# Performance work log

Measured on AMD Instinct MI355X. Metric: run time of the kernel, lower is better.

Reference implementation:

```python
import jax, jax.numpy as jnp
import numpy as np
from jax import lax

N_QUBITS = 10
N_LAYERS = 6
DIM = 1 << N_QUBITS
EPS = 1e-5

_i = np.arange(DIM)
# Z_SIGNS[w, i] = (+1/-1) eigenvalue of PauliZ on wire w (wire 0 = most significant bit)
Z_SIGNS = jnp.asarray(np.stack([1.0 - 2.0 * ((_i >> (N_QUBITS - 1 - w)) & 1) for w in range(N_QUBITS)]).astype(np.float32))

def _layer_perm(r):
    # composed permutation of the ring of CNOT(w, (w+r)%n) gates of one StronglyEntanglingLayers layer
    p = _i.copy()
    for w in range(N_QUBITS):
        c, t = w, (w + r) % N_QUBITS
        pc, pt = N_QUBITS - 1 - c, N_QUBITS - 1 - t
        pg = _i ^ (((_i >> pc) & 1) << pt)
        p = p[pg]
    return p

LAYER_PERMS = [jnp.asarray(_layer_perm(l % (N_QUBITS - 1) + 1), dtype=jnp.int32) for l in range(N_LAYERS)]

def _apply_1q(state, U, wire):
    # state: (B, DIM) complex64; U: (2,2) or batched (B,2,2)
    B = state.shape[0]
    left = 1 << wire
    right = DIM // (2 * left)
    s = state.reshape(B, left, 2, right)
    if U.ndim == 3:
        out = jnp.einsum('bij,bljr->blir', U, s)
    else:
        out = jnp.einsum('ij,bljr->blir', U, s)
    return out.reshape(B, DIM)

def _ry_batched(theta):
    c = jnp.cos(theta / 2)
    s = jnp.sin(theta / 2)
    return jnp.stack([jnp.stack([c, -s], -1), jnp.stack([s, c], -1)], -2).astype(jnp.complex64)

def _rot(phi, theta, omega):
    # PennyLane Rot(phi, theta, omega) = RZ(omega) @ RY(theta) @ RZ(phi)
    c = jnp.cos(theta / 2)
    s = jnp.sin(theta / 2)
    m00 = jnp.exp(-1j * (phi + omega) / 2) * c
    m01 = -jnp.exp(1j * (phi - omega) / 2) * s
    m10 = jnp.exp(-1j * (phi - omega) / 2) * s
    m11 = jnp.exp(1j * (phi + omega) / 2) * c
    return jnp.stack([jnp.stack([m00, m01]), jnp.stack([m10, m11])]).astype(jnp.complex64)

def quantum_forward(xq, qw):
    # batched statevector simulation of: RY(pi*x_i) encoding + StronglyEntanglingLayers
    B = xq.shape[0]
    state = jnp.zeros((B, DIM), jnp.complex64).at[:, 0].set(1.0)
    for w in range(N_QUBITS):
        state = _apply_1q(state, _ry_batched(jnp.pi * xq[:, w]), w)
    for l in range(N_LAYERS):
        for w in range(N_QUBITS):
            state = _apply_1q(state, _rot(qw[l, w, 0], qw[l, w, 1], qw[l, w, 2]), w)
        state = state[:, LAYER_PERMS[l]]
    probs = state.real ** 2 + state.imag ** 2
    return probs @ Z_SIGNS.T  # (B, N_QUBITS) expvals of PauliZ

def _conv(x, w, b):
    y = lax.conv_general_dilated(x, w, (1, 1), 'SAME', dimension_numbers=('NCHW', 'OIHW', 'NCHW'))
    return y + b[None, :, None, None]

def _bn(x, g, b):
    # BatchNorm2d in training mode: per-batch statistics over (N, H, W)
    m = jnp.mean(x, (0, 2, 3), keepdims=True)
    v = jnp.var(x, (0, 2, 3), keepdims=True)
    return (x - m) * lax.rsqrt(v + EPS) * g[None, :, None, None] + b[None, :, None, None]

def _pool(x):
    return lax.reduce_window(x, -jnp.inf, lax.max, (1, 1, 2, 2), (1, 1, 2, 2), 'VALID')

def setup_inputs() -> dict:
    key = jax.random.key(0)
    ks = jax.random.split(key, 16)
    n = lambda k, sh, sc: jax.random.normal(k, sh, jnp.float32) * sc
    return {
        'x': jax.random.normal(ks[0], (256, 3, 64, 64), jnp.float32),
        'conv1_w': n(ks[1], (32, 3, 3, 3), 0.1), 'conv1_b': jnp.zeros(32),
        'bn1_g': jnp.ones(32), 'bn1_b': jnp.zeros(32),
        'conv2_w': n(ks[2], (32, 32, 3, 3), 0.05), 'conv2_b': jnp.zeros(32),
        'bn2_g': jnp.ones(32), 'bn2_b': jnp.zeros(32),
        'conv3_w': n(ks[3], (64, 32, 3, 3), 0.05), 'conv3_b': jnp.zeros(64),
        'bn3_g': jnp.ones(64), 'bn3_b': jnp.zeros(64),
        'conv4_w': n(ks[4], (64, 64, 3, 3), 0.05), 'conv4_b': jnp.zeros(64),
        'bn4_g': jnp.ones(64), 'bn4_b': jnp.zeros(64),
        'fc1_w': n(ks[5], (128, 64 * 16 * 16), 0.01), 'fc1_b': jnp.zeros(128),
        'fc2_w': n(ks[6], (10, 128), 0.05), 'fc2_b': jnp.zeros(10),
        'q_weights': jax.random.uniform(ks[7], (6, 10, 3), jnp.float32),
        'head_w': n(ks[8], (10, 10), 0.1), 'head_b': jnp.zeros(10),
    }

def reference(x, conv1_w, conv1_b, bn1_g, bn1_b, conv2_w, conv2_b, bn2_g, bn2_b,
              conv3_w, conv3_b, bn3_g, bn3_b, conv4_w, conv4_b, bn4_g, bn4_b,
              fc1_w, fc1_b, fc2_w, fc2_b, q_weights, head_w, head_b):
    h = jax.nn.relu(_bn(_conv(x, conv1_w, conv1_b), bn1_g, bn1_b))
    h = jax.nn.relu(_bn(_conv(h, conv2_w, conv2_b), bn2_g, bn2_b))
    h = _pool(h)  # Dropout(0.25) is identity in eval
    h = jax.nn.relu(_bn(_conv(h, conv3_w, conv3_b), bn3_g, bn3_b))
    h = jax.nn.relu(_bn(_conv(h, conv4_w, conv4_b), bn4_g, bn4_b))
    h = _pool(h)
    h = h.reshape(h.shape[0], -1)  # (B, 64*16*16)
    h = jax.nn.relu(h @ fc1_w.T + fc1_b)
    h = h @ fc2_w.T + fc2_b  # (B, n_qubits)
    q = quantum_forward(h, q_weights)
    return q @ head_w.T + head_b  # (B, num_classes)
```

## Files before the change

kernel.cpp:

```cpp
#include <hip/hip_runtime.h>
#include <math.h>

#define PI_F 3.14159265358979323846f

typedef __attribute__((ext_vector_type(8))) _Float16 half8;
typedef __attribute__((ext_vector_type(4))) _Float16 half4;
typedef __attribute__((ext_vector_type(4))) float f32x4;

__global__ __launch_bounds__(256) void x_to_nhwc4_kernel(
    const float* __restrict__ x, _Float16* __restrict__ X4)
{
    int idx = blockIdx.x * 256 + threadIdx.x;
    int n = idx >> 11;
    int p = (idx & 2047) * 2;
    const float* xb = x + (size_t)n * 12288;
    float2 c0 = *(const float2*)&xb[p];
    float2 c1 = *(const float2*)&xb[4096 + p];
    float2 c2 = *(const float2*)&xb[8192 + p];
    half8 o;
    o[0] = (_Float16)c0.x; o[1] = (_Float16)c1.x; o[2] = (_Float16)c2.x; o[3] = (_Float16)0.f;
    o[4] = (_Float16)c0.y; o[5] = (_Float16)c1.y; o[6] = (_Float16)c2.y; o[7] = (_Float16)0.f;
    *(half8*)&X4[(size_t)idx * 8] = o;
}

__global__ __launch_bounds__(256) void wt_transform_kernel(
    const float* __restrict__ w1, const float* __restrict__ w2,
    const float* __restrict__ w3, const float* __restrict__ w4,
    _Float16* __restrict__ t1, _Float16* __restrict__ t2,
    _Float16* __restrict__ t3, _Float16* __restrict__ t4)
{
    int idx = blockIdx.x * 256 + threadIdx.x;
    if (idx < 9216) {
        int j = idx & 7, co = (idx >> 3) & 31, k8 = idx >> 8;
        int k = k8 * 8 + j, tap = k >> 5, ci = k & 31;
        t2[idx] = (_Float16)w2[(size_t)(co * 32 + ci) * 9 + tap];
    } else if (idx < 27648) {
        int e = idx - 9216;
        int j = e & 7, co = (e >> 3) & 31, r = e >> 8;
        int k8 = r % 36, gg = r / 36;
        int k = k8 * 8 + j, tap = k >> 5, ci = k & 31;
        t3[e] = (_Float16)w3[(size_t)((gg * 32 + co) * 32 + ci) * 9 + tap];
    } else if (idx < 64512) {
        int e = idx - 27648;
        int j = e & 7, co = (e >> 3) & 31, r = e >> 8;
        int k8 = r % 36, gc = r / 36;
        int g = gc >> 1, cc = gc & 1;
        int kl = k8 * 8 + j, tap = kl >> 5, ci = cc * 32 + (kl & 31);
        t4[e] = (_Float16)w4[(size_t)((g * 32 + co) * 64 + ci) * 9 + tap];
    } else if (idx < 66560) {
        int e = idx - 64512;
        int j = e & 7, co = (e >> 3) & 31, k8 = e >> 8;
        int k = k8 * 8 + j, tap = k >> 2, ci = k & 3;
        t1[e] = (_Float16)((tap < 9 && ci < 3) ? w1[(size_t)(co * 3 + ci) * 9 + tap] : 0.f);
    }
}

__global__ __launch_bounds__(256) void fc1w_transform_kernel(
    const float* __restrict__ w, _Float16* __restrict__ wt)
{
    __shared__ float lds[64][65];
    const int t = threadIdx.x;
    const int yx0 = blockIdx.x * 64;
    const int j = blockIdx.y;
    #pragma unroll
    for (int i = 0; i < 16; ++i) {
        int idx = t + 256 * i;
        int c = idx >> 6, yxl = idx & 63;
        lds[c][yxl] = w[(size_t)j * 16384 + c * 256 + yx0 + yxl];
    }
    __syncthreads();
    #pragma unroll
    for (int i = 0; i < 2; ++i) {
        int idx = t + 256 * i;
        int yxl = idx >> 3, c8 = idx & 7;
        half8 h;
        #pragma unroll
        for (int jj = 0; jj < 8; ++jj)
            h[jj] = (_Float16)lds[c8 * 8 + jj][yxl];
        *(half8*)&wt[(size_t)j * 16384 + (size_t)(yx0 + yxl) * 64 + c8 * 8] = h;
    }
}

__global__ __launch_bounds__(256) void quantum_prep_kernel(
    const float* __restrict__ qw, float* __restrict__ rotm,
    unsigned short* __restrict__ perm)
{
    int t = threadIdx.x;
    if (t < 60) {
        float phi = qw[t * 3], th = qw[t * 3 + 1], om = qw[t * 3 + 2];
        float c = cosf(0.5f * th), s = sinf(0.5f * th);
        float apo = 0.5f * (phi + om), amo = 0.5f * (phi - om);
        float cpo = cosf(apo), spo = sinf(apo);
        float cmo = cosf(amo), smo = sinf(amo);
        rotm[t * 8 + 0] = cpo * c;  rotm[t * 8 + 1] = -spo * c;
        rotm[t * 8 + 2] = -cmo * s; rotm[t * 8 + 3] = -smo * s;
        rotm[t * 8 + 4] = cmo * s;  rotm[t * 8 + 5] = -smo * s;
        rotm[t * 8 + 6] = cpo * c;  rotm[t * 8 + 7] = spo * c;
    }
    for (int e = t; e < 6144; e += 256) {
        int layer = e >> 10, i = e & 1023;
        int r = layer % 9 + 1;
        int jdx = i;
        for (int w = 9; w >= 0; --w) {
            int tt = (w + r) % 10;
            int pc = 9 - w, pt_ = 9 - tt;
            jdx ^= ((jdx >> pc) & 1) << pt_;
        }
        perm[e] = (unsigned short)jdx;
    }
}

__global__ __launch_bounds__(256) void conv1_mfma_kernel(
    const _Float16* __restrict__ X4, const _Float16* __restrict__ w1m,
    const float* __restrict__ bias, _Float16* __restrict__ out,
    float* __restrict__ partials)
{
    constexpr int TC = 66, TR = 6;
    constexpr int NPIX = (TR + 1) * TC;
    __shared__ __align__(16) _Float16 s_in[NPIX * 4];
    __shared__ __align__(16) _Float16 s_w[2048];
    __shared__ float s_red[64];

    const int t = threadIdx.x;
    const int row0 = blockIdx.x * 4;
    const int n = blockIdx.z;

    *(half8*)&s_w[t * 8] = *(const half8*)&w1m[t * 8];

    for (int p = t; p < NPIX; p += 256) {
        int col = p % TC, r = p / TC;
        int gy = row0 + r - 1, gx = col - 1;
        uint2 u = make_uint2(0u, 0u);
        if (r < TR && gy >= 0 && gy < 64 && gx >= 0 && gx < 64)
            u = *(const uint2*)&X4[(((size_t)n << 12) + (gy << 6) + gx) * 4];
        *(uint2*)&s_in[p * 4] = u;
    }
    if (t < 64) s_red[t] = 0.f;
    __syncthreads();

    const int w = t >> 6, l = t & 63;
    const int lm = l & 15, lg = l >> 4;
    int pA[4];
    #pragma unroll
    for (int f = 0; f < 4; ++f) {
        int m = w * 64 + f * 16 + lm;
        pA[f] = (m >> 6) * TC + (m & 63);
    }
    f32x4 zero4 = {0.f, 0.f, 0.f, 0.f};
    f32x4 acc[4][2];
    #pragma unroll
    for (int f = 0; f < 4; ++f) { acc[f][0] = zero4; acc[f][1] = zero4; }

    {
        const int t0 = lg * 2;
        const int off0 = (t0 / 3) * TC + (t0 % 3);
        const int off1 = ((t0 + 1) / 3) * TC + ((t0 + 1) % 3);
        half8 b0 = *(const half8*)&s_w[(lg * 32 + lm) * 8];
        half8 b1 = *(const half8*)&s_w[(lg * 32 + 16 + lm) * 8];
        #pragma unroll
        for (int f = 0; f < 4; ++f) {
            half4 alo = *(const half4*)&s_in[(pA[f] + off0) * 4];
            half4 ahi = *(const half4*)&s_in[(pA[f] + off1) * 4];
            half8 a;
            #pragma unroll
            for (int j = 0; j < 4; ++j) { a[j] = alo[j]; a[4 + j] = ahi[j]; }
            acc[f][0] = __builtin_amdgcn_mfma_f32_16x16x32_f16(a, b0, acc[f][0], 0, 0, 0);
            acc[f][1] = __builtin_amdgcn_mfma_f32_16x16x32_f16(a, b1, acc[f][1], 0, 0, 0);
        }
    }
    {
        half8 b0 = *(const half8*)&s_w[((4 + lg) * 32 + lm) * 8];
        half8 b1 = *(const half8*)&s_w[((4 + lg) * 32 + 16 + lm) * 8];
        #pragma unroll
        for (int f = 0; f < 4; ++f) {
            half8 a;
            #pragma unroll
            for (int j = 0; j < 8; ++j) a[j] = (_Float16)0.f;
            if (lg == 0) {
                half4 alo = *(const half4*)&s_in[(pA[f] + 134) * 4];
                half4 ahi = *(const half4*)&s_in[(pA[f] + 198) * 4];
                #pragma unroll
                for (int j = 0; j < 4; ++j) { a[j] = alo[j]; a[4 + j] = ahi[j]; }
            }
            acc[f][0] = __builtin_amdgcn_mfma_f32_16x16x32_f16(a, b0, acc[f][0], 0, 0, 0);
            acc[f][1] = __builtin_amdgcn_mfma_f32_16x16x32_f16(a, b1, acc[f][1], 0, 0, 0);
        }
    }

    float bv0 = bias[lm];
    float bv1 = bias[16 + lm];
    float s0 = 0.f, s20 = 0.f, s1 = 0.f, s21 = 0.f;
    #pragma unroll
    for (int f = 0; f < 4; ++f) {
        #pragma unroll
        for (int r = 0; r < 4; ++r) {
            int m = w * 64 + f * 16 + lg * 4 + r;
            int yy = row0 + (m >> 6), xo = m & 63;
            size_t base = (((size_t)n * 64 + yy) * 64 + xo) * 32;
            float v0 = acc[f][0][r] + bv0;
            float v1 = acc[f][1][r] + bv1;
            out[base + lm] = (_Float16)v0;
            out[base + 16 + lm] = (_Float16)v1;
            s0 += v0; s20 += v0 * v0;
            s1 += v1; s21 += v1 * v1;
        }
    }
    s0 += __shfl_xor(s0, 16);  s0 += __shfl_xor(s0, 32);
    s1 += __shfl_xor(s1, 16);  s1 += __shfl_xor(s1, 32);
    s20 += __shfl_xor(s20, 16); s20 += __shfl_xor(s20, 32);
    s21 += __shfl_xor(s21, 16); s21 += __shfl_xor(s21, 32);
    if (l < 16) {
        atomicAdd(&s_red[lm], s0);
        atomicAdd(&s_red[16 + lm], s1);
        atomicAdd(&s_red[32 + lm], s20);
        atomicAdd(&s_red[48 + lm], s21);
    }
    __syncthreads();
    if (t < 64)
        partials[((size_t)n * 16 + blockIdx.x) * 64 + t] = s_red[t];
}

template<int BLOCK, int W, int CIN, int COUT, int NCH, int MF, int NB,
         bool MMIN, bool POOL>
__global__ __launch_bounds__(BLOCK, (BLOCK == 512 ? 4 : 3)) void conv_mfma_kernel(
    const _Float16* __restrict__ in0, const _Float16* __restrict__ in1,
    const _Float16* __restrict__ coef, const _Float16* __restrict__ wt,
    const float* __restrict__ bias,
    _Float16* __restrict__ out0, _Float16* __restrict__ out1,
    float* __restrict__ partials)
{
    constexpr int H = W;
    constexpr int NWAVE = BLOCK / 64;
    constexpr int SPW = MF * 16;
    constexpr int ROWS = NWAVE * SPW / W;
    constexpr int TR = ROWS + 2;
    constexpr int TC = W + 2;
    constexpr int NPIX = TR * TC;
    constexpr int CCI = 32;
    constexpr int KC = 9 * CCI;
    constexpr int COUTB = NB * 16;
    __shared__ __align__(16) _Float16 s_in[NPIX * CCI];
    __shared__ float s_red[2 * COUTB];

    const int t = threadIdx.x;
    const int row0 = blockIdx.x * ROWS;
    const int n = blockIdx.z;

    const int w = t >> 6, l = t & 63;
    const int lm = l & 15, lg = l >> 4;
    int pA[MF];
    #pragma unroll
    for (int f = 0; f < MF; ++f) {
        int m = w * SPW + f * 16 + lm;
        pA[f] = (m / W) * TC + (m % W);
    }
    f32x4 zero4 = {0.f, 0.f, 0.f, 0.f};
    f32x4 acc[MF][NB];
    #pragma unroll
    for (int f = 0; f < MF; ++f)
        #pragma unroll
        for (int nb = 0; nb < NB; ++nb) acc[f][nb] = zero4;
    if (t < 2 * COUTB) s_red[t] = 0.f;

    #pragma unroll
    for (int cc = 0; cc < NCH; ++cc) {
        __syncthreads();
        for (int idx = t; idx < NPIX * 4; idx += BLOCK) {
            int c8 = idx & 3;
            int p = idx >> 2;
            int col = p % TC, r = p / TC;
            int gy = row0 + r - 1, gx = col - 1;
            half8 v;
            #pragma unroll
            for (int j = 0; j < 8; ++j) v[j] = (_Float16)0.f;
            if (gy >= 0 && gy < H && gx >= 0 && gx < W) {
                size_t gidx = (((size_t)n * H + gy) * W + gx) * CIN + cc * CCI + c8 * 8;
                if (MMIN) {
                    half8 mn = *(const half8*)&in0[gidx];
                    half8 mx = *(const half8*)&in1[gidx];
                    half8 sa = *(const half8*)&coef[cc * CCI + c8 * 8];
                    half8 sb = *(const half8*)&coef[CIN + cc * CCI + c8 * 8];
                    half8 sh = *(const half8*)&coef[2 * CIN + cc * CCI + c8 * 8];
                    #pragma unroll
                    for (int j = 0; j < 8; ++j) {
                        _Float16 f = mx[j] * sa[j] + mn[j] * sb[j] + sh[j];
                        v[j] = f > (_Float16)0.f ? f : (_Float16)0.f;
                    }
                } else {
                    v = *(const half8*)&in0[gidx];
                    if (coef) {
                        half8 sc = *(const half8*)&coef[cc * CCI + c8 * 8];
                        half8 sh = *(const half8*)&coef[CIN + cc * CCI + c8 * 8];
                        #pragma unroll
                        for (int j = 0; j < 8; ++j) {
                            _Float16 f = v[j] * sc[j] + sh[j];
                            v[j] = f > (_Float16)0.f ? f : (_Float16)0.f;
                        }
                    }
                }
            }
            *(half8*)&s_in[(c8 * NPIX + p) * 8] = v;
        }
        __syncthreads();
        #pragma unroll
        for (int tap = 0; tap < 9; ++tap) {
            const int dy = tap / 3, dx = tap % 3;
            const int poff = dy * TC + dx;
            half8 b[NB];
            #pragma unroll
            for (int nb = 0; nb < NB; ++nb) {
                int cog = nb * 16 + lm;
                int gg = cog >> 5, col = cog & 31;
                const _Float16* wp = wt + (size_t)(gg * NCH + cc) * KC * 32;
                b[nb] = *(const half8*)&wp[((tap * 4 + lg) * 32 + col) * 8];
            }
            #pragma unroll
            for (int f = 0; f < MF; ++f) {
                half8 a = *(const half8*)&s_in[(lg * NPIX + pA[f] + poff) * 8];
                #pragma unroll
                for (int nb = 0; nb < NB; ++nb)
                    acc[f][nb] = __builtin_amdgcn_mfma_f32_16x16x32_f16(a, b[nb], acc[f][nb], 0, 0, 0);
            }
        }
    }

    float bv[NB], s[NB], s2[NB];
    #pragma unroll
    for (int nb = 0; nb < NB; ++nb) {
        bv[nb] = bias[nb * 16 + lm];
        s[nb] = 0.f; s2[nb] = 0.f;
    }
    #pragma unroll
    for (int f = 0; f < MF; ++f) {
        #pragma unroll
        for (int r = 0; r < 4; ++r) {
            int m = w * SPW + f * 16 + lg * 4 + r;
            int yy = row0 + m / W, xo = m % W;
            size_t base = (((size_t)n * H + yy) * W + xo) * COUT;
            #pragma unroll
            for (int nb = 0; nb < NB; ++nb) {
                float v = acc[f][nb][r] + bv[nb];
                if (!POOL) out0[base + nb * 16 + lm] = (_Float16)v;
                s[nb] += v; s2[nb] += v * v;
            }
        }
    }
    #pragma unroll
    for (int nb = 0; nb < NB; ++nb) {
        s[nb] += __shfl_xor(s[nb], 16);  s[nb] += __shfl_xor(s[nb], 32);
        s2[nb] += __shfl_xor(s2[nb], 16); s2[nb] += __shfl_xor(s2[nb], 32);
    }
    if (l < 16) {
        #pragma unroll
        for (int nb = 0; nb < NB; ++nb) {
            atomicAdd(&s_red[nb * 16 + lm], s[nb]);
            atomicAdd(&s_red[COUTB + nb * 16 + lm], s2[nb]);
        }
    }

    if (POOL) {
        constexpr int FH = MF / 2;
        const int yp = (row0 >> 1) + w;
        #pragma unroll
        for (int nb = 0; nb < NB; ++nb) {
            #pragma unroll
            for (int f = 0; f < FH; ++f) {
                #pragma unroll
                for (int rp = 0; rp < 2; ++rp) {
                    float a0 = acc[f][nb][2 * rp] + bv[nb];
                    float a1 = acc[f][nb][2 * rp + 1] + bv[nb];
                    float a2 = acc[f + FH][nb][2 * rp] + bv[nb];
                    float a3 = acc[f + FH][nb][2 * rp + 1] + bv[nb];
                    float mn = fminf(fminf(a0, a1), fminf(a2, a3));
                    float mx = fmaxf(fmaxf(a0, a1), fmaxf(a2, a3));
                    int xp = f * 8 + lg * 2 + rp;
                    size_t ob = (((size_t)n * (W / 2) + yp) * (W / 2) + xp) * COUT
                                + nb * 16 + lm;
                    out0[ob] = (_Float16)mn;
                    out1[ob] = (_Float16)mx;
                }
            }
        }
    }

    __syncthreads();
    if (t < 2 * COUTB) {
        size_t bid = (size_t)n * gridDim.x + blockIdx.x;
        partials[bid * 2 * COUTB + t] = s_red[t];
    }
}

__global__ __launch_bounds__(256) void bn_finalize_kernel(
    const float* __restrict__ partials, int nx, float inv_count,
    const float* __restrict__ gamma, const float* __restrict__ beta,
    float* __restrict__ ss, _Float16* __restrict__ ssh,
    _Float16* __restrict__ sab, int COUT)
{
    const int c = blockIdx.x;
    const int t = threadIdx.x;
    float sum = 0.f, sq = 0.f;
    int total = 256 * nx;
    for (int e = t; e < total; e += 256) {
        size_t off = (size_t)e * 2 * COUT;
        sum += partials[off + c];
        sq  += partials[off + COUT + c];
    }
    #pragma unroll
    for (int off = 32; off > 0; off >>= 1) {
        sum += __shfl_xor(sum, off);
        sq  += __shfl_xor(sq, off);
    }
    __shared__ float rs[4], rq[4];
    if ((t & 63) == 0) { rs[t >> 6] = sum; rq[t >> 6] = sq; }
    __syncthreads();
    if (t == 0) {
        sum = rs[0] + rs[1] + rs[2] + rs[3];
        sq  = rq[0] + rq[1] + rq[2] + rq[3];
        float mean = sum * inv_count;
        float var = sq * inv_count - mean * mean;
        float scale = gamma[c] * rsqrtf(var + 1e-5f);
        float shift = beta[c] - mean * scale;
        ss[c] = scale;
        ss[COUT + c] = shift;
        if (ssh) {
            ssh[c] = (_Float16)scale;
            ssh[COUT + c] = (_Float16)shift;
        }
        if (sab) {
            sab[c] = (_Float16)(scale > 0.f ? scale : 0.f);
            sab[COUT + c] = (_Float16)(scale > 0.f ? 0.f : scale);
            sab[2 * COUT + c] = (_Float16)shift;
        }
    }
}

__global__ __launch_bounds__(256) void fc1_mfma_kernel(
    const _Float16* __restrict__ Amin, const _Float16* __restrict__ Amax,
    const _Float16* __restrict__ sab, const _Float16* __restrict__ Bw,
    float* __restrict__ hp)
{
    __shared__ __align__(16) _Float16 As[64][72];
    __shared__ __align__(16) _Float16 Bs[128][72];
    const int t = threadIdx.x;
    const int mt = blockIdx.x;
    const int kc = blockIdx.y;
    const int w = t >> 6, l = t & 63;
    const int lm = l & 15, lg = l >> 4;

    f32x4 zero4 = {0.f, 0.f, 0.f, 0.f};
    f32x4 acc[8];
    #pragma unroll
    for (int nb = 0; nb < 8; ++nb) acc[nb] = zero4;

    const size_t a_base = (size_t)(mt * 64) * 16384 + (size_t)kc * 512;
    const size_t b_base = (size_t)kc * 512;

    for (int p = 0; p < 8; ++p) {
        __syncthreads();
        #pragma unroll
        for (int i = 0; i < 2; ++i) {
            int idx = t + 256 * i;
            int r = idx >> 3, c8 = idx & 7;
            size_t off = a_base + (size_t)r * 16384 + p * 64 + c8 * 8;
            half8 mn = *(const half8*)&Amin[off];
            half8 mx = *(const half8*)&Amax[off];
            half8 sa = *(const half8*)&sab[c8 * 8];
            half8 sb = *(const half8*)&sab[64 + c8 * 8];
            half8 sh = *(const half8*)&sab[128 + c8 * 8];
            half8 v;
            #pragma unroll
            for (int j = 0; j < 8; ++j) {
                _Float16 f = mx[j] * sa[j] + mn[j] * sb[j] + sh[j];
                v[j] = f > (_Float16)0.f ? f : (_Float16)0.f;
            }
            *(half8*)&As[r][c8 * 8] = v;
        }
        #pragma unroll
        for (int i = 0; i < 4; ++i) {
            int idx = t + 256 * i;
            int r = idx >> 3, c8 = idx & 7;
            *(half8*)&Bs[r][c8 * 8] =
                *(const half8*)&Bw[b_base + (size_t)r * 16384 + p * 64 + c8 * 8];
        }
        __syncthreads();
        #pragma unroll
        for (int ks = 0; ks < 64; ks += 32) {
            half8 a = *(const half8*)&As[w * 16 + lm][ks + lg * 8];
            #pragma unroll
            for (int nb = 0; nb < 8; ++nb) {
                half8 b = *(const half8*)&Bs[nb * 16 + lm][ks + lg * 8];
                acc[nb] = __builtin_amdgcn_mfma_f32_16x16x32_f16(a, b, acc[nb], 0, 0, 0);
            }
        }
    }
    #pragma unroll
    for (int nb = 0; nb < 8; ++nb) {
        #pragma unroll
        for (int r = 0; r < 4; ++r) {
            int row = mt * 64 + w * 16 + lg * 4 + r;
            hp[((size_t)kc * 256 + row) * 128 + nb * 16 + lm] = acc[nb][r];
        }
    }
}

__global__ __launch_bounds__(256) void fc1_reduce_kernel(
    const float* __restrict__ hp, const float* __restrict__ bias, float* __restrict__ h1)
{
    int gid = blockIdx.x * 256 + threadIdx.x;
    int n = gid >> 7, j = gid & 127;
    float s = bias[j];
    #pragma unroll
    for (int kc = 0; kc < 32; ++kc) s += hp[((size_t)kc * 256 + n) * 128 + j];
    h1[gid] = fmaxf(0.f, s);
}

__global__ __launch_bounds__(64) void fc2_kernel(
    const float* __restrict__ h1, const float* __restrict__ w,
    const float* __restrict__ b, float* __restrict__ xq)
{
    int n = blockIdx.x, l = threadIdx.x;
    float a0 = h1[n * 128 + l], a1 = h1[n * 128 + 64 + l];
    float p[10];
    #pragma unroll
    for (int j = 0; j < 10; ++j)
        p[j] = w[j * 128 + l] * a0 + w[j * 128 + 64 + l] * a1;
    #pragma unroll
    for (int j = 0; j < 10; ++j) {
        #pragma unroll
        for (int off = 32; off > 0; off >>= 1) p[j] += __shfl_xor(p[j], off);
    }
    if (l == 0) {
        #pragma unroll
        for (int j = 0; j < 10; ++j) xq[n * 10 + j] = p[j] + b[j];
    }
}

__global__ __launch_bounds__(64) void quantum_head_kernel(
    const float* __restrict__ xq, const float* __restrict__ rotm,
    const unsigned short* __restrict__ perm,
    const float* __restrict__ head_w, const float* __restrict__ head_b,
    float* __restrict__ outp)
{
    __shared__ float lds[2048];
    const int n = blockIdx.x;
    const int l = threadIdx.x;

    float ar[16], ai[16];
    #pragma unroll
    for (int r = 0; r < 16; ++r) { ar[r] = 0.f; ai[r] = 0.f; }
    if (l == 0) ar[0] = 1.f;

    #pragma unroll
    for (int w = 0; w < 10; ++w) {
        float th = 0.5f * PI_F * xq[n * 10 + w];
        float c = cosf(th), s = sinf(th);
        const int k = 9 - w;
        if (k >= 6) {
            const int b = k - 6;
            #pragma unroll
            for (int r = 0; r < 16; ++r) {
                if (!(r & (1 << b))) {
                    int r1 = r | (1 << b);
                    float a0 = ar[r], a1 = ar[r1];
                    ar[r]  = c * a0 - s * a1;
                    ar[r1] = s * a0 + c * a1;
                }
            }
        } else {
            float ss = ((l >> k) & 1) ? s : -s;
            #pragma unroll
            for (int r = 0; r < 16; ++r) {
                float p = __shfl_xor(ar[r], 1 << k);
                ar[r] = c * ar[r] + ss * p;
            }
        }
    }

    #pragma unroll 1
    for (int layer = 0; layer < 6; ++layer) {
        #pragma unroll
        for (int w = 0; w < 10; ++w) {
            const float* m = rotm + (layer * 10 + w) * 8;
            float m00r = m[0], m00i = m[1], m01r = m[2], m01i = m[3];
            float m10r = m[4], m10i = m[5], m11r = m[6], m11i = m[7];
            const int k = 9 - w;
            if (k >= 6) {
                const int b = k - 6;
                #pragma unroll
                for (int r = 0; r < 16; ++r) {
                    if (!(r & (1 << b))) {
                        int r1 = r | (1 << b);
                        float a0r = ar[r], a0i = ai[r];
                        float a1r = ar[r1], a1i = ai[r1];
                        ar[r]  = m00r * a0r - m00i * a0i + m01r * a1r - m01i * a1i;
                        ai[r]  = m00r * a0i + m00i * a0r + m01r * a1i + m01i * a1r;
                        ar[r1] = m10r * a0r - m10i * a0i + m11r * a1r - m11i * a1i;
                        ai[r1] = m10r * a0i + m10i * a0r + m11r * a1i + m11i * a1r;
                    }
                }
            } else {
                int bit = (l >> k) & 1;
                float mAr = bit ? m11r : m00r, mAi = bit ? m11i : m00i;
                float mBr = bit ? m10r : m01r, mBi = bit ? m10i : m01i;
                #pragma unroll
                for (int r = 0; r < 16; ++r) {
                    float pr = __shfl_xor(ar[r], 1 << k);
                    float pi = __shfl_xor(ai[r], 1 << k);
                    float mr = ar[r], mi = ai[r];
                    ar[r] = mAr * mr - mAi * mi + mBr * pr - mBi * pi;
                    ai[r] = mAr * mi + mAi * mr + mBr * pi + mBi * pr;
                }
            }
        }
        #pragma unroll
        for (int r = 0; r < 16; ++r) {
            lds[(r << 6) | l] = ar[r];
            lds[1024 + ((r << 6) | l)] = ai[r];
        }
        __syncthreads();
        const unsigned short* pt = perm + layer * 1024;
        #pragma unroll
        for (int r = 0; r < 16; ++r) {
            int ji = pt[(r << 6) | l];
            ar[r] = lds[ji];
            ai[r] = lds[1024 + ji];
        }
        __syncthreads();
    }

    float S = 0.f, T0 = 0.f, T1 = 0.f, T2 = 0.f, T3 = 0.f;
    #pragma unroll
    for (int r = 0; r < 16; ++r) {
        float pr = ar[r] * ar[r] + ai[r] * ai[r];
        S += pr;
        T0 += (r & 1) ? -pr : pr;
        T1 += (r & 2) ? -pr : pr;
        T2 += (r & 4) ? -pr : pr;
        T3 += (r & 8) ? -pr : pr;
    }
    float pk[10];
    pk[0] = T3; pk[1] = T2; pk[2] = T1; pk[3] = T0;
    #pragma unroll
    for (int w = 4; w < 10; ++w)
        pk[w] = ((l >> (9 - w)) & 1) ? -S : S;
    #pragma unroll
    for (int w = 0; w < 10; ++w) {
        #pragma unroll
        for (int off = 1; off < 64; off <<= 1)
            pk[w] += __shfl_xor(pk[w], off);
    }
    if (l < 10) {
        float o = head_b[l];
        #pragma unroll
        for (int kk = 0; kk < 10; ++kk) o += pk[kk] * head_w[l * 10 + kk];
        outp[n * 10 + l] = o;
    }
}

extern "C" void kernel_launch(void* const* d_in, const int* in_sizes, int n_in,
                              void* d_out, int out_size, void* d_ws, size_t ws_size,
                              hipStream_t stream)
{
    const float* x   = (const float*)d_in[0];
    const float* c1w = (const float*)d_in[1];  const float* c1b = (const float*)d_in[2];
    const float* g1  = (const float*)d_in[3];  const float* b1  = (const float*)d_in[4];
    const float* c2w = (const float*)d_in[5];  const float* c2b = (const float*)d_in[6];
    const float* g2  = (const float*)d_in[7];  const float* b2  = (const float*)d_in[8];
    const float* c3w = (const float*)d_in[9];  const float* c3b = (const float*)d_in[10];
    const float* g3  = (const float*)d_in[11]; const float* b3  = (const float*)d_in[12];
    const float* c4w = (const float*)d_in[13]; const float* c4b = (const float*)d_in[14];
    const float* g4  = (const float*)d_in[15]; const float* b4  = (const float*)d_in[16];
    const float* f1w = (const float*)d_in[17]; const float* f1b = (const float*)d_in[18];
    const float* f2w = (const float*)d_in[19]; const float* f2b = (const float*)d_in[20];
    const float* qw  = (const float*)d_in[21];
    const float* hw  = (const float*)d_in[22]; const float* hb  = (const float*)d_in[23];

    float* ws = (float*)d_ws;
    _Float16* H0 = (_Float16*)ws;
    _Float16* H1 = H0 + 33554432;
    float* part = ws + 33554432;
    float* ss1  = part + 524288;
    float* ss2  = ss1 + 64;
    float* ss3  = ss2 + 64;
    float* ss4  = ss3 + 128;
    float* hp   = ss4 + 128;
    float* h1   = hp + 1048576;
    float* xqv  = h1 + 32768;
    float* rotm = xqv + 2560;
    unsigned short* perm16 = (unsigned short*)(rotm + 480);
    _Float16* ssh1 = (_Float16*)(perm16 + 6144);
    _Float16* ssh3 = ssh1 + 64;
    _Float16* sab2 = ssh3 + 128;
    _Float16* sab4 = sab2 + 96;
    _Float16* wt2  = sab4 + 192;
    _Float16* wt3  = wt2 + 9216;
    _Float16* wt4  = wt3 + 18432;
    _Float16* w1m  = wt4 + 36864;
    _Float16* w1t  = w1m + 2048;
    _Float16* X4   = w1t + 2097152;

    _Float16* minT2 = H1;
    _Float16* maxT2 = H1 + 8388608;
    _Float16* minT4 = H1;
    _Float16* maxT4 = H1 + 4194304;

    quantum_prep_kernel<<<1, 256, 0, stream>>>(qw, rotm, perm16);
    wt_transform_kernel<<<260, 256, 0, stream>>>(c1w, c2w, c3w, c4w, w1m, wt2, wt3, wt4);
    fc1w_transform_kernel<<<dim3(4, 128), 256, 0, stream>>>(f1w, w1t);
    x_to_nhwc4_kernel<<<2048, 256, 0, stream>>>(x, X4);

    conv1_mfma_kernel<<<dim3(16, 1, 256), 256, 0, stream>>>(X4, w1m, c1b, H0, part);
    bn_finalize_kernel<<<32, 256, 0, stream>>>(part, 16, 1.f / 1048576.f,
                                               g1, b1, ss1, ssh1, nullptr, 32);

    conv_mfma_kernel<256, 64, 32, 32, 1, 8, 2, false, true>
        <<<dim3(8, 1, 256), 256, 0, stream>>>(
        H0, nullptr, ssh1, wt2, c2b, minT2, maxT2, part);
    bn_finalize_kernel<<<32, 256, 0, stream>>>(part, 8, 1.f / 1048576.f,
                                               g2, b2, ss2, nullptr, sab2, 32);

    conv_mfma_kernel<512, 32, 32, 64, 1, 4, 4, true, false>
        <<<dim3(2, 1, 256), 512, 0, stream>>>(
        minT2, maxT2, sab2, wt3, c3b, H0, nullptr, part);
    bn_finalize_kernel<<<64, 256, 0, stream>>>(part, 2, 1.f / 262144.f,
                                               g3, b3, ss3, ssh3, nullptr, 64);

    conv_mfma_kernel<512, 32, 64, 64, 2, 4, 4, false, true>
        <<<dim3(2, 1, 256), 512, 0, stream>>>(
        H0, nullptr, ssh3, wt4, c4b, minT4, maxT4, part);
    bn_finalize_kernel<<<64, 256, 0, stream>>>(part, 2, 1.f / 262144.f,
                                               g4, b4, ss4, nullptr, sab4, 64);

    fc1_mfma_kernel<<<dim3(4, 32), 256, 0, stream>>>(minT4, maxT4, sab4, w1t, hp);
    fc1_reduce_kernel<<<128, 256, 0, stream>>>(hp, f1b, h1);

    fc2_kernel<<<256, 64, 0, stream>>>(h1, f2w, f2b, xqv);

    quantum_head_kernel<<<256, 64, 0, stream>>>(xqv, rotm, perm16, hw, hb, (float*)d_out);
}
```

Measured before the change: 220.8 us.

## Stage all input channels once per conv block and coalesce pooled output stores via LDS

The conv kernel now loads every input channel of the halo tile into shared memory in a single pass, instead of looping over 32-channel chunks with a barrier pair per chunk. The MFMA loop is reordered to iterate taps then channel chunks. For pooled layers, min/max results are first packed into shared memory and then written out as contiguous half8 vectors, replacing scattered 2-byte global stores. The cost is more LDS per block for the CIN=64 case (conv4), which may lower occupancy, plus an extra barrier pair for the pooling pack.

```diff
diff --git a/kernel.cpp b/kernel.cpp
--- a/kernel.cpp
+++ b/kernel.cpp
@@ -220,7 +220,7 @@
         partials[((size_t)n * 16 + blockIdx.x) * 64 + t] = s_red[t];
 }
 
-template<int BLOCK, int W, int CIN, int COUT, int NCH, int MF, int NB,
+template<int BLOCK, int W, int CIN, int COUT, int MF, int NB,
          bool MMIN, bool POOL>
 __global__ __launch_bounds__(BLOCK, (BLOCK == 512 ? 4 : 3)) void conv_mfma_kernel(
     const _Float16* __restrict__ in0, const _Float16* __restrict__ in1,
@@ -236,10 +236,11 @@
     constexpr int TR = ROWS + 2;
     constexpr int TC = W + 2;
     constexpr int NPIX = TR * TC;
-    constexpr int CCI = 32;
-    constexpr int KC = 9 * CCI;
+    constexpr int NCH = CIN / 32;
+    constexpr int C8N = CIN / 8;
+    constexpr int KC = 288;
     constexpr int COUTB = NB * 16;
-    __shared__ __align__(16) _Float16 s_in[NPIX * CCI];
+    __shared__ __align__(16) _Float16 s_in[NPIX * CIN];
     __shared__ float s_red[2 * COUTB];
 
     const int t = threadIdx.x;
@@ -262,50 +263,50 @@
         for (int nb = 0; nb < NB; ++nb) acc[f][nb] = zero4;
     if (t < 2 * COUTB) s_red[t] = 0.f;
 
-    #pragma unroll
-    for (int cc = 0; cc < NCH; ++cc) {
-        __syncthreads();
-        for (int idx = t; idx < NPIX * 4; idx += BLOCK) {
-            int c8 = idx & 3;
-            int p = idx >> 2;
-            int col = p % TC, r = p / TC;
-            int gy = row0 + r - 1, gx = col - 1;
-            half8 v;
-            #pragma unroll
-            for (int j = 0; j < 8; ++j) v[j] = (_Float16)0.f;
-            if (gy >= 0 && gy < H && gx >= 0 && gx < W) {
-                size_t gidx = (((size_t)n * H + gy) * W + gx) * CIN + cc * CCI + c8 * 8;
-                if (MMIN) {
-                    half8 mn = *(const half8*)&in0[gidx];
-                    half8 mx = *(const half8*)&in1[gidx];
-                    half8 sa = *(const half8*)&coef[cc * CCI + c8 * 8];
-                    half8 sb = *(const half8*)&coef[CIN + cc * CCI + c8 * 8];
-                    half8 sh = *(const half8*)&coef[2 * CIN + cc * CCI + c8 * 8];
+    for (int idx = t; idx < NPIX * C8N; idx += BLOCK) {
+        int c8 = idx % C8N;
+        int p = idx / C8N;
+        int col = p % TC, r = p / TC;
+        int gy = row0 + r - 1, gx = col - 1;
+        half8 v;
+        #pragma unroll
+        for (int j = 0; j < 8; ++j) v[j] = (_Float16)0.f;
+        if (gy >= 0 && gy < H && gx >= 0 && gx < W) {
+            size_t gidx = (((size_t)n * H + gy) * W + gx) * CIN + c8 * 8;
+            if (MMIN) {
+                half8 mn = *(const half8*)&in0[gidx];
+                half8 mx = *(const half8*)&in1[gidx];
+                half8 sa = *(const half8*)&coef[c8 * 8];
+                half8 sb = *(const half8*)&coef[CIN + c8 * 8];
+                half8 sh = *(const half8*)&coef[2 * CIN + c8 * 8];
+                #pragma unroll
+                for (int j = 0; j < 8; ++j) {
+                    _Float16 f = mx[j] * sa[j] + mn[j] * sb[j] + sh[j];
+                    v[j] = f > (_Float16)0.f ? f : (_Float16)0.f;
+                }
+            } else {
+                v = *(const half8*)&in0[gidx];
+                if (coef) {
+                    half8 sc = *(const half8*)&coef[c8 * 8];
+                    half8 sh = *(const half8*)&coef[CIN + c8 * 8];
                     #pragma unroll
                     for (int j = 0; j < 8; ++j) {
-                        _Float16 f = mx[j] * sa[j] + mn[j] * sb[j] + sh[j];
+                        _Float16 f = v[j] * sc[j] + sh[j];
                         v[j] = f > (_Float16)0.f ? f : (_Float16)0.f;
                     }
-                } else {
-                    v = *(const half8*)&in0[gidx];
-                    if (coef) {
-                        half8 sc = *(const half8*)&coef[cc * CCI + c8 * 8];
-                        half8 sh = *(const half8*)&coef[CIN + cc * CCI + c8 * 8];
-                        #pragma unroll
-                        for (int j = 0; j < 8; ++j) {
-                            _Float16 f = v[j] * sc[j] + sh[j];
-                            v[j] = f > (_Float16)0.f ? f : (_Float16)0.f;
-                        }
-                    }
                 }
             }
-            *(half8*)&s_in[(c8 * NPIX + p) * 8] = v;
-        }
-        __syncthreads();
-        #pragma unroll
-        for (int tap = 0; tap < 9; ++tap) {
-            const int dy = tap / 3, dx = tap % 3;
-            const int poff = dy * TC + dx;
+        }
+        *(half8*)&s_in[(c8 * NPIX + p) * 8] = v;
+    }
+    __syncthreads();
+
+    #pragma unroll
+    for (int tap = 0; tap < 9; ++tap) {
+        const int dy = tap / 3, dx = tap % 3;
+        const int poff = dy * TC + dx;
+        #pragma unroll
+        for (int cc = 0; cc < NCH; ++cc) {
             half8 b[NB];
             #pragma unroll
             for (int nb = 0; nb < NB; ++nb) {
@@ -316,7 +317,7 @@
             }
             #pragma unroll
             for (int f = 0; f < MF; ++f) {
-                half8 a = *(const half8*)&s_in[(lg * NPIX + pA[f] + poff) * 8];
+                half8 a = *(const half8*)&s_in[((cc * 4 + lg) * NPIX + pA[f] + poff) * 8];
                 #pragma unroll
                 for (int nb = 0; nb < NB; ++nb)
                     acc[f][nb] = __builtin_amdgcn_mfma_f32_16x16x32_f16(a, b[nb], acc[f][nb], 0, 0, 0);
@@ -360,7 +361,10 @@
 
     if (POOL) {
         constexpr int FH = MF / 2;
-        const int yp = (row0 >> 1) + w;
+        constexpr int PPIX = (ROWS / 2) * (W / 2);
+        static_assert(2 * PPIX * COUT <= NPIX * CIN, "pool pack fits in s_in");
+        __syncthreads();
+        _Float16* pk = s_in;
         #pragma unroll
         for (int nb = 0; nb < NB; ++nb) {
             #pragma unroll
@@ -374,12 +378,17 @@
                     float mn = fminf(fminf(a0, a1), fminf(a2, a3));
                     float mx = fmaxf(fmaxf(a0, a1), fmaxf(a2, a3));
                     int xp = f * 8 + lg * 2 + rp;
-                    size_t ob = (((size_t)n * (W / 2) + yp) * (W / 2) + xp) * COUT
-                                + nb * 16 + lm;
-                    out0[ob] = (_Float16)mn;
-                    out1[ob] = (_Float16)mx;
+                    int o = (w * (W / 2) + xp) * COUT + nb * 16 + lm;
+                    pk[o] = (_Float16)mn;
+                    pk[PPIX * COUT + o] = (_Float16)mx;
                 }
             }
+        }
+        __syncthreads();
+        size_t gb = (((size_t)n * (H / 2) + (row0 >> 1)) * (W / 2)) * COUT;
+        for (int idx = t; idx < PPIX * COUT / 8; idx += BLOCK) {
+            *(half8*)&out0[gb + (size_t)idx * 8] = *(const half8*)&pk[idx * 8];
+            *(half8*)&out1[gb + (size_t)idx * 8] = *(const half8*)&pk[(PPIX * COUT + idx * 8)];
         }
     }
 
@@ -713,19 +722,19 @@
     bn_finalize_kernel<<<32, 256, 0, stream>>>(part, 16, 1.f / 1048576.f,
                                                g1, b1, ss1, ssh1, nullptr, 32);
 
-    conv_mfma_kernel<256, 64, 32, 32, 1, 8, 2, false, true>
+    conv_mfma_kernel<256, 64, 32, 32, 8, 2, false, true>
         <<<dim3(8, 1, 256), 256, 0, stream>>>(
         H0, nullptr, ssh1, wt2, c2b, minT2, maxT2, part);
     bn_finalize_kernel<<<32, 256, 0, stream>>>(part, 8, 1.f / 1048576.f,
                                                g2, b2, ss2, nullptr, sab2, 32);
 
-    conv_mfma_kernel<512, 32, 32, 64, 1, 4, 4, true, false>
+    conv_mfma_kernel<512, 32, 32, 64, 4, 4, true, false>
         <<<dim3(2, 1, 256), 512, 0, stream>>>(
         minT2, maxT2, sab2, wt3, c3b, H0, nullptr, part);
     bn_finalize_kernel<<<64, 256, 0, stream>>>(part, 2, 1.f / 262144.f,
                                                g3, b3, ss3, ssh3, nullptr, 64);
 
-    conv_mfma_kernel<512, 32, 64, 64, 2, 4, 4, false, true>
+    conv_mfma_kernel<512, 32, 64, 64, 4, 4, false, true>
         <<<dim3(2, 1, 256), 512, 0, stream>>>(
         H0, nullptr, ssh3, wt4, c4b, minT4, maxT4, part);
     bn_finalize_kernel<<<64, 256, 0, stream>>>(part, 2, 1.f / 262144.f,
```

Result: faster. 203.0 us (-8.1%).
